# Kernel optimization log

Measured on AMD Instinct MI355X. Metric: run time of the kernel, lower is better.

Reference implementation:

```python
import jax, jax.numpy as jnp
import numpy as np

B, S, D_IN = 4, 2048, 1024
EMBED, HEADS = 1024, 16
HEAD_DIM = EMBED // HEADS


def setup_inputs() -> dict:
    key = jax.random.key(0)
    k1, k2, k3 = jax.random.split(key, 3)
    x = jax.random.normal(k1, (B, S, D_IN), dtype=jnp.float32)
    # xavier-uniform-ish init scales
    lim_qkv = float(np.sqrt(6.0 / (D_IN + 3 * EMBED)))
    lim_o = float(np.sqrt(6.0 / (EMBED + EMBED)))
    w_qkv = jax.random.uniform(k2, (3 * EMBED, D_IN), minval=-lim_qkv, maxval=lim_qkv, dtype=jnp.float32)
    b_qkv = jnp.zeros((3 * EMBED,), dtype=jnp.float32)
    w_o = jax.random.uniform(k3, (EMBED, EMBED), minval=-lim_o, maxval=lim_o, dtype=jnp.float32)
    b_o = jnp.zeros((EMBED,), dtype=jnp.float32)
    return {"x": x, "w_qkv": w_qkv, "b_qkv": b_qkv, "w_o": w_o, "b_o": b_o}


def reference(x, w_qkv, b_qkv, w_o, b_o):
    b, s, _ = x.shape
    qkv = jnp.einsum('bsi,oi->bso', x, w_qkv) + b_qkv            # (b, s, 3E)
    qkv = qkv.reshape(b, s, HEADS, 3 * HEAD_DIM).transpose(0, 2, 1, 3)  # (b, h, s, 3d)
    q, k, v = jnp.split(qkv, 3, axis=-1)                          # each (b, h, s, d)
    scale = 1.0 / jnp.sqrt(jnp.float32(HEAD_DIM))
    attn = jnp.einsum('bhqd,bhkd->bhqk', q, k) * scale            # (b, h, s, s)
    attn = jax.nn.softmax(attn, axis=-1)
    vals = jnp.einsum('bhqk,bhkd->bhqd', attn, v)                 # (b, h, s, d)
    # NOTE: original torch code reshapes (b,h,s,d) -> (b,s,e) WITHOUT transposing
    # heads back; jnp.reshape reproduces that flattening exactly.
    vals = vals.reshape(b, s, EMBED)
    out = jnp.einsum('bse,oe->bso', vals, w_o) + b_o              # (b, s, E)
    return out
```

## Files before the change

kernel.cpp:

```cpp
#include <hip/hip_runtime.h>
#include <stdint.h>
#include <stddef.h>

#define DEVINL __device__ __forceinline__

typedef unsigned short u16;
typedef unsigned int u32;
typedef __attribute__((ext_vector_type(8))) short short8;
typedef __attribute__((ext_vector_type(4))) float f32x4;
typedef __attribute__((ext_vector_type(4))) u32 u32x4;
typedef __attribute__((ext_vector_type(2))) u32 u32x2;

#define QSCALE 0.18033688011112042f

DEVINL u16 f2bf(float f) {
    u32 u = __builtin_bit_cast(u32, f);
    u32 r = (u + 0x7fffu + ((u >> 16) & 1u)) >> 16;
    return (u16)r;
}

DEVINL void gld_lds16(const void* g, void* l) {
    __builtin_amdgcn_global_load_lds(
        (__attribute__((address_space(1))) u32*)(uintptr_t)g,
        (__attribute__((address_space(3))) u32*)l, 16, 0, 0);
}

DEVINL u32 pack_bf16_trunc(float lo, float hi) {
    return __builtin_amdgcn_perm(__builtin_bit_cast(u32, hi),
                                 __builtin_bit_cast(u32, lo), 0x07060302u);
}

__global__ void prep_inputs(const float* __restrict__ x, const float* __restrict__ wqkv,
                            const float* __restrict__ bqkv, const float* __restrict__ wo,
                            u16* __restrict__ xb, u16* __restrict__ wqb,
                            u16* __restrict__ wob, float* __restrict__ bsc) {
    int blk = blockIdx.x;
    if (blk < 6144) {
        const float* src; u16* dst; int base; bool qscale = false;
        if (blk < 4096)      { src = x;    dst = xb;  base = blk; }
        else if (blk < 5632) { src = wqkv; dst = wqb; base = blk - 4096; qscale = true; }
        else                 { src = wo;   dst = wob; base = blk - 5632; }
        int i = (base * 256 + threadIdx.x) * 8;
        float sc = 1.0f;
        if (qscale) { int row = i >> 10; if ((row % 192) < 64) sc = QSCALE; }
        float4 a = *(const float4*)(src + i);
        float4 c = *(const float4*)(src + i + 4);
        union { u16 s[8]; u32x4 v; } t;
        t.s[0] = f2bf(a.x * sc); t.s[1] = f2bf(a.y * sc); t.s[2] = f2bf(a.z * sc); t.s[3] = f2bf(a.w * sc);
        t.s[4] = f2bf(c.x * sc); t.s[5] = f2bf(c.y * sc); t.s[6] = f2bf(c.z * sc); t.s[7] = f2bf(c.w * sc);
        *(u32x4*)(dst + i) = t.v;
    } else {
        int i = (blk - 6144) * 256 + threadIdx.x;
        float sc = ((i % 192) < 64) ? QSCALE : 1.0f;
        bsc[i] = bqkv[i] * sc;
    }
}

__global__ void gemm_qkv(const u16* __restrict__ A, const u16* __restrict__ Bm,
                         const float* __restrict__ bias, u16* __restrict__ qkvb,
                         u16* __restrict__ vtb) {
    const int K = 1024, N = 3072;
    __shared__ u16 As[128 * 32];
    __shared__ u16 Bs[128 * 32];
    const int tid = threadIdx.x;
    const int lane = tid & 63;
    const int wv = tid >> 6, wr = wv >> 1, wc = wv & 1;
    const int l15 = lane & 15, quad = lane >> 4;
    const int m0 = blockIdx.y * 128, n0 = blockIdx.x * 128;

    f32x4 acc[4][4];
#pragma unroll
    for (int i = 0; i < 4; i++)
#pragma unroll
        for (int j = 0; j < 4; j++) acc[i][j] = (f32x4){0.f, 0.f, 0.f, 0.f};

    const u16* Ab = A + (size_t)m0 * K;
    const u16* Bb = Bm + (size_t)n0 * K;
    const int srow = tid >> 2;
    const int sc8 = (tid & 3) * 8;

    for (int k0 = 0; k0 < K; k0 += 32) {
#pragma unroll
        for (int i = 0; i < 2; i++) {
            int row = i * 64 + srow;
            gld_lds16(Ab + (size_t)row * K + k0 + sc8, (char*)As + (size_t)(i * 256 + tid) * 16);
            gld_lds16(Bb + (size_t)row * K + k0 + sc8, (char*)Bs + (size_t)(i * 256 + tid) * 16);
        }
        __syncthreads();
        short8 af[4], bf8[4];
#pragma unroll
        for (int mi = 0; mi < 4; mi++)
            af[mi] = *(const short8*)(As + (wr * 64 + mi * 16 + l15) * 32 + quad * 8);
#pragma unroll
        for (int ni = 0; ni < 4; ni++)
            bf8[ni] = *(const short8*)(Bs + (wc * 64 + ni * 16 + l15) * 32 + quad * 8);
#pragma unroll
        for (int mi = 0; mi < 4; mi++)
#pragma unroll
            for (int ni = 0; ni < 4; ni++)
                acc[mi][ni] = __builtin_amdgcn_mfma_f32_16x16x32_bf16(af[mi], bf8[ni], acc[mi][ni], 0, 0, 0);
        __syncthreads();
    }

#pragma unroll
    for (int mi = 0; mi < 4; mi++) {
        int row_b = m0 + wr * 64 + mi * 16 + quad * 4;
#pragma unroll
        for (int ni = 0; ni < 4; ni++) {
            int c0 = n0 + wc * 64 + ni * 16;
            int sec0 = c0 % 192;
            float bv = bias[c0 + l15];
            float v0 = acc[mi][ni][0] + bv;
            float v1 = acc[mi][ni][1] + bv;
            float v2 = acc[mi][ni][2] + bv;
            float v3 = acc[mi][ni][3] + bv;
            if (sec0 >= 128) {
                int hh = c0 / 192;
                int b = row_b >> 11;
                int s = row_b & 2047;
                int d = sec0 - 128 + l15;
                u32 lo = (u32)f2bf(v0) | ((u32)f2bf(v1) << 16);
                u32 hi = (u32)f2bf(v2) | ((u32)f2bf(v3) << 16);
                *(u32x2*)(vtb + ((size_t)((b * 16 + hh) * 64 + d)) * 2048 + s) = (u32x2){lo, hi};
            } else {
                int col = c0 + l15;
                qkvb[(size_t)(row_b + 0) * N + col] = f2bf(v0);
                qkvb[(size_t)(row_b + 1) * N + col] = f2bf(v1);
                qkvb[(size_t)(row_b + 2) * N + col] = f2bf(v2);
                qkvb[(size_t)(row_b + 3) * N + col] = f2bf(v3);
            }
        }
    }
}

__global__ void gemm_out(const u16* __restrict__ A, const u16* __restrict__ Bm,
                         const float* __restrict__ bias, float* __restrict__ C) {
    const int K = 1024, N = 1024;
    __shared__ u16 As[128 * 32];
    __shared__ u16 Bs[64 * 32];
    const int tid = threadIdx.x;
    const int lane = tid & 63;
    const int wv = tid >> 6, wr = wv >> 1, wc = wv & 1;
    const int l15 = lane & 15, quad = lane >> 4;
    const int m0 = blockIdx.y * 128, n0 = blockIdx.x * 64;

    f32x4 acc[4][2];
#pragma unroll
    for (int i = 0; i < 4; i++)
#pragma unroll
        for (int j = 0; j < 2; j++) acc[i][j] = (f32x4){0.f, 0.f, 0.f, 0.f};

    const u16* Ab = A + (size_t)m0 * K;
    const u16* Bb = Bm + (size_t)n0 * K;
    const int srow = tid >> 2;
    const int sc8 = (tid & 3) * 8;

    for (int k0 = 0; k0 < K; k0 += 32) {
#pragma unroll
        for (int i = 0; i < 2; i++)
            gld_lds16(Ab + (size_t)(i * 64 + srow) * K + k0 + sc8, (char*)As + (size_t)(i * 256 + tid) * 16);
        gld_lds16(Bb + (size_t)srow * K + k0 + sc8, (char*)Bs + (size_t)tid * 16);
        __syncthreads();
        short8 af[4], bf8[2];
#pragma unroll
        for (int mi = 0; mi < 4; mi++)
            af[mi] = *(const short8*)(As + (wr * 64 + mi * 16 + l15) * 32 + quad * 8);
#pragma unroll
        for (int ni = 0; ni < 2; ni++)
            bf8[ni] = *(const short8*)(Bs + (wc * 32 + ni * 16 + l15) * 32 + quad * 8);
#pragma unroll
        for (int mi = 0; mi < 4; mi++)
#pragma unroll
            for (int ni = 0; ni < 2; ni++)
                acc[mi][ni] = __builtin_amdgcn_mfma_f32_16x16x32_bf16(af[mi], bf8[ni], acc[mi][ni], 0, 0, 0);
        __syncthreads();
    }

#pragma unroll
    for (int mi = 0; mi < 4; mi++) {
        int row_b = m0 + wr * 64 + mi * 16 + quad * 4;
#pragma unroll
        for (int ni = 0; ni < 2; ni++) {
            int col = n0 + wc * 32 + ni * 16 + l15;
            float bv = bias[col];
#pragma unroll
            for (int r = 0; r < 4; r++)
                C[(size_t)(row_b + r) * N + col] = acc[mi][ni][r] + bv;
        }
    }
}

__launch_bounds__(256, 4)
__global__ void flash_attn(const u16* __restrict__ qkv, const u16* __restrict__ vt,
                           u16* __restrict__ vals2) {
    __shared__ u16 Ks[64 * 72];
    __shared__ u16 Vts[64 * 72];
    __shared__ u16 Ps[4][32 * 72];

    const int tid = threadIdx.x;
    const int lane = tid & 63, wv = tid >> 6;
    const int l15 = lane & 15, quad = lane >> 4;
    const int s0 = blockIdx.x * 128;
    const int bh = blockIdx.y, b = bh >> 4, h = bh & 15;

    short8 qf[2][2];
    const u16* qbase = qkv + (size_t)(b * 2048 + s0 + wv * 32) * 3072 + h * 192;
#pragma unroll
    for (int qi = 0; qi < 2; qi++)
#pragma unroll
        for (int ks = 0; ks < 2; ks++)
            qf[qi][ks] = *(const short8*)(qbase + (size_t)(qi * 16 + l15) * 3072 + ks * 32 + quad * 8);

    f32x4 o_acc[2][4];
    f32x4 sum_acc[2];
#pragma unroll
    for (int qi = 0; qi < 2; qi++) {
        sum_acc[qi] = (f32x4){0.f, 0.f, 0.f, 0.f};
#pragma unroll
        for (int nd = 0; nd < 4; nd++) o_acc[qi][nd] = (f32x4){0.f, 0.f, 0.f, 0.f};
    }

    const u16* kg = qkv + (size_t)(b * 2048) * 3072 + h * 192 + 64;
    const u16* vg = vt + (size_t)bh * 64 * 2048;
    const int srow = tid >> 2;
    const int sc16 = (tid & 3) * 16;

    const short8 ones = (short8){0x3F80, 0x3F80, 0x3F80, 0x3F80, 0x3F80, 0x3F80, 0x3F80, 0x3F80};

    for (int kb = 0; kb < 2048; kb += 64) {
        __syncthreads();
        u32x4 k0 = *(const u32x4*)(kg + (size_t)(kb + srow) * 3072 + sc16);
        u32x4 k1 = *(const u32x4*)(kg + (size_t)(kb + srow) * 3072 + sc16 + 8);
        u32x4 v0 = *(const u32x4*)(vg + (size_t)srow * 2048 + kb + sc16);
        u32x4 v1 = *(const u32x4*)(vg + (size_t)srow * 2048 + kb + sc16 + 8);
        *(u32x4*)(Ks + srow * 72 + sc16) = k0;
        *(u32x4*)(Ks + srow * 72 + sc16 + 8) = k1;
        *(u32x4*)(Vts + srow * 72 + sc16) = v0;
        *(u32x4*)(Vts + srow * 72 + sc16 + 8) = v1;
        __syncthreads();

        f32x4 s_acc[4][2];
#pragma unroll
        for (int ki = 0; ki < 4; ki++)
#pragma unroll
            for (int qi = 0; qi < 2; qi++) s_acc[ki][qi] = (f32x4){0.f, 0.f, 0.f, 0.f};
#pragma unroll
        for (int ki = 0; ki < 4; ki++) {
#pragma unroll
            for (int ks = 0; ks < 2; ks++) {
                short8 kf = *(const short8*)(Ks + (ki * 16 + l15) * 72 + ks * 32 + quad * 8);
#pragma unroll
                for (int qi = 0; qi < 2; qi++)
                    s_acc[ki][qi] = __builtin_amdgcn_mfma_f32_16x16x32_bf16(kf, qf[qi][ks], s_acc[ki][qi], 0, 0, 0);
            }
        }

#pragma unroll
        for (int ki = 0; ki < 4; ki++)
#pragma unroll
            for (int qi = 0; qi < 2; qi++) {
                float p0 = __builtin_amdgcn_exp2f(s_acc[ki][qi][0]);
                float p1 = __builtin_amdgcn_exp2f(s_acc[ki][qi][1]);
                float p2 = __builtin_amdgcn_exp2f(s_acc[ki][qi][2]);
                float p3 = __builtin_amdgcn_exp2f(s_acc[ki][qi][3]);
                u32x2 pk = (u32x2){pack_bf16_trunc(p0, p1), pack_bf16_trunc(p2, p3)};
                *(u32x2*)(Ps[wv] + (qi * 16 + l15) * 72 + ki * 16 + quad * 4) = pk;
            }

#pragma unroll
        for (int c = 0; c < 2; c++) {
            short8 ap[2];
#pragma unroll
            for (int qi = 0; qi < 2; qi++)
                ap[qi] = *(const short8*)(Ps[wv] + (qi * 16 + l15) * 72 + c * 32 + quad * 8);
#pragma unroll
            for (int qi = 0; qi < 2; qi++)
                sum_acc[qi] = __builtin_amdgcn_mfma_f32_16x16x32_bf16(ap[qi], ones, sum_acc[qi], 0, 0, 0);
#pragma unroll
            for (int nd = 0; nd < 4; nd++) {
                short8 bv = *(const short8*)(Vts + (nd * 16 + l15) * 72 + c * 32 + quad * 8);
#pragma unroll
                for (int qi = 0; qi < 2; qi++)
                    o_acc[qi][nd] = __builtin_amdgcn_mfma_f32_16x16x32_bf16(ap[qi], bv, o_acc[qi][nd], 0, 0, 0);
            }
        }
    }

#pragma unroll
    for (int qi = 0; qi < 2; qi++) {
        f32x4 inv;
#pragma unroll
        for (int r = 0; r < 4; r++) inv[r] = 1.0f / sum_acc[qi][r];
#pragma unroll
        for (int nd = 0; nd < 4; nd++) {
            int d = nd * 16 + l15;
#pragma unroll
            for (int r = 0; r < 4; r++) {
                int s = s0 + wv * 32 + qi * 16 + quad * 4 + r;
                size_t row2 = (size_t)(b * 2048 + h * 128 + (s >> 4));
                int col2 = ((s & 15) << 6) + d;
                vals2[row2 * 1024 + col2] = f2bf(o_acc[qi][nd][r] * inv[r]);
            }
        }
    }
}

extern "C" void kernel_launch(void* const* d_in, const int* in_sizes, int n_in,
                              void* d_out, int out_size, void* d_ws, size_t ws_size,
                              hipStream_t stream) {
    (void)in_sizes; (void)n_in; (void)out_size; (void)ws_size;
    const float* x      = (const float*)d_in[0];
    const float* w_qkv  = (const float*)d_in[1];
    const float* b_qkv  = (const float*)d_in[2];
    const float* w_o    = (const float*)d_in[3];
    const float* b_o    = (const float*)d_in[4];
    float* out = (float*)d_out;

    char* ws = (char*)d_ws;
    u16* xb   = (u16*)(ws);
    u16* wqb  = (u16*)(ws + 16777216);
    u16* wob  = (u16*)(ws + 23068672);
    u16* qkvb = (u16*)(ws + 25165824);
    u16* vtb  = (u16*)(ws + 75497472);
    u16* v2b  = (u16*)(ws + 92274688);
    float* bsc = (float*)(ws + 92274688);

    prep_inputs<<<6156, 256, 0, stream>>>(x, w_qkv, b_qkv, w_o, xb, wqb, wob, bsc);

    gemm_qkv<<<dim3(24, 64), 256, 0, stream>>>(xb, wqb, bsc, qkvb, vtb);

    flash_attn<<<dim3(16, 64), 256, 0, stream>>>(qkvb, vtb, v2b);

    gemm_out<<<dim3(16, 64), 256, 0, stream>>>(v2b, wob, b_o, out);
}
```

Before: 279.8 us.

## Load K/V tiles via direct global-to-LDS loads with XOR-swizzled layout

Replaces register-staged global loads and LDS stores of the K and V^T tiles in flash attention with global_load_lds direct transfers. Because those direct loads write contiguously, the padded stride-72 LDS layout is replaced by an unpadded stride-64 layout with an XOR swizzle on 8-element groups, applied consistently to K, V and P reads and writes to avoid bank conflicts. This cuts VGPR use and LDS footprint and removes the store instructions, at the cost of extra index arithmetic and the risk that the swizzle does not fully remove conflicts on the P writes.

Measured after the change: 269.7 us. -3.6%, faster.

```diff
diff --git a/kernel.cpp b/kernel.cpp
--- a/kernel.cpp
+++ b/kernel.cpp
@@ -193,13 +193,14 @@
 __launch_bounds__(256, 4)
 __global__ void flash_attn(const u16* __restrict__ qkv, const u16* __restrict__ vt,
                            u16* __restrict__ vals2) {
-    __shared__ u16 Ks[64 * 72];
-    __shared__ u16 Vts[64 * 72];
-    __shared__ u16 Ps[4][32 * 72];
+    __shared__ u16 Ks[64 * 64];
+    __shared__ u16 Vts[64 * 64];
+    __shared__ u16 Ps[4][32 * 64];
 
     const int tid = threadIdx.x;
     const int lane = tid & 63, wv = tid >> 6;
     const int l15 = lane & 15, quad = lane >> 4;
+    const int e7 = (l15 & 7) * 8;
     const int s0 = blockIdx.x * 128;
     const int bh = blockIdx.y, b = bh >> 4, h = bh & 15;
 
@@ -222,21 +223,23 @@
 
     const u16* kg = qkv + (size_t)(b * 2048) * 3072 + h * 192 + 64;
     const u16* vg = vt + (size_t)bh * 64 * 2048;
-    const int srow = tid >> 2;
-    const int sc16 = (tid & 3) * 16;
+
+    const int lrow = lane >> 3;
+    const int lgr  = (lane & 7) ^ lrow;
+    const int r0   = wv * 8 + lrow;
 
     const short8 ones = (short8){0x3F80, 0x3F80, 0x3F80, 0x3F80, 0x3F80, 0x3F80, 0x3F80, 0x3F80};
 
     for (int kb = 0; kb < 2048; kb += 64) {
         __syncthreads();
-        u32x4 k0 = *(const u32x4*)(kg + (size_t)(kb + srow) * 3072 + sc16);
-        u32x4 k1 = *(const u32x4*)(kg + (size_t)(kb + srow) * 3072 + sc16 + 8);
-        u32x4 v0 = *(const u32x4*)(vg + (size_t)srow * 2048 + kb + sc16);
-        u32x4 v1 = *(const u32x4*)(vg + (size_t)srow * 2048 + kb + sc16 + 8);
-        *(u32x4*)(Ks + srow * 72 + sc16) = k0;
-        *(u32x4*)(Ks + srow * 72 + sc16 + 8) = k1;
-        *(u32x4*)(Vts + srow * 72 + sc16) = v0;
-        *(u32x4*)(Vts + srow * 72 + sc16 + 8) = v1;
+#pragma unroll
+        for (int j = 0; j < 2; j++) {
+            int row = j * 32 + r0;
+            gld_lds16(kg + (size_t)(kb + row) * 3072 + lgr * 8,
+                      (char*)Ks + (size_t)(j * 256 + tid) * 16);
+            gld_lds16(vg + (size_t)row * 2048 + kb + lgr * 8,
+                      (char*)Vts + (size_t)(j * 256 + tid) * 16);
+        }
         __syncthreads();
 
         f32x4 s_acc[4][2];
@@ -248,7 +251,7 @@
         for (int ki = 0; ki < 4; ki++) {
 #pragma unroll
             for (int ks = 0; ks < 2; ks++) {
-                short8 kf = *(const short8*)(Ks + (ki * 16 + l15) * 72 + ks * 32 + quad * 8);
+                short8 kf = *(const short8*)(Ks + (ki * 16 + l15) * 64 + ((ks * 32 + quad * 8) ^ e7));
 #pragma unroll
                 for (int qi = 0; qi < 2; qi++)
                     s_acc[ki][qi] = __builtin_amdgcn_mfma_f32_16x16x32_bf16(kf, qf[qi][ks], s_acc[ki][qi], 0, 0, 0);
@@ -264,7 +267,7 @@
                 float p2 = __builtin_amdgcn_exp2f(s_acc[ki][qi][2]);
                 float p3 = __builtin_amdgcn_exp2f(s_acc[ki][qi][3]);
                 u32x2 pk = (u32x2){pack_bf16_trunc(p0, p1), pack_bf16_trunc(p2, p3)};
-                *(u32x2*)(Ps[wv] + (qi * 16 + l15) * 72 + ki * 16 + quad * 4) = pk;
+                *(u32x2*)(Ps[wv] + (qi * 16 + l15) * 64 + ((ki * 16 + quad * 4) ^ e7)) = pk;
             }
 
 #pragma unroll
@@ -272,13 +275,13 @@
             short8 ap[2];
 #pragma unroll
             for (int qi = 0; qi < 2; qi++)
-                ap[qi] = *(const short8*)(Ps[wv] + (qi * 16 + l15) * 72 + c * 32 + quad * 8);
+                ap[qi] = *(const short8*)(Ps[wv] + (qi * 16 + l15) * 64 + ((c * 32 + quad * 8) ^ e7));
 #pragma unroll
             for (int qi = 0; qi < 2; qi++)
                 sum_acc[qi] = __builtin_amdgcn_mfma_f32_16x16x32_bf16(ap[qi], ones, sum_acc[qi], 0, 0, 0);
 #pragma unroll
             for (int nd = 0; nd < 4; nd++) {
-                short8 bv = *(const short8*)(Vts + (nd * 16 + l15) * 72 + c * 32 + quad * 8);
+                short8 bv = *(const short8*)(Vts + (nd * 16 + l15) * 64 + ((c * 32 + quad * 8) ^ e7));
 #pragma unroll
                 for (int qi = 0; qi < 2; qi++)
                     o_acc[qi][nd] = __builtin_amdgcn_mfma_f32_16x16x32_bf16(ap[qi], bv, o_acc[qi][nd], 0, 0, 0);
```
